# Performance work log

Measured on AMD Instinct MI355X. Metric: run time of the kernel, lower is better.

## Reference

```python
import jax, jax.numpy as jnp
import numpy as np

N_E = 8192
E_DIM = 512
BETA = 0.25


def setup_inputs() -> dict:
    key = jax.random.key(0)
    k1, k2, k3, k4, k5 = jax.random.split(key, 5)
    B, C, T = 8, E_DIM, 1024
    z = jax.random.normal(k1, (B, C, T), dtype=jnp.float32)
    # domain ids: 0 (speech), 1 (music), 2 (audio), 3 (no restriction / else-branch)
    audio_domain = jax.random.randint(k2, (B,), 0, 4, dtype=jnp.int64)
    # frozen codebook, init N(0, e_dim^-0.5) as in nn.init.normal_
    emb_weight = jax.random.normal(k3, (N_E, E_DIM), dtype=jnp.float32) * (E_DIM ** -0.5)
    # embedding_proj = nn.Linear(e_dim, e_dim): weight [out,in], bias [out]
    lim = 1.0 / np.sqrt(E_DIM)
    proj_w = jax.random.uniform(k4, (E_DIM, E_DIM), minval=-lim, maxval=lim, dtype=jnp.float32)
    proj_b = jax.random.uniform(k5, (E_DIM,), minval=-lim, maxval=lim, dtype=jnp.float32)
    return {"z": z, "audio_domain": audio_domain, "n_q": 1,
            "emb_weight": emb_weight, "proj_w": proj_w, "proj_b": proj_b}


def _domain_valid_mask(audio_domain):
    # valid[b, n] = True if code n is allowed for sample b
    cs = N_E // 4
    idx = jnp.arange(N_E)                      # [n_e]
    dom = audio_domain[:, None]                # [B, 1]
    m0 = idx < cs                              # domain 0: first quarter
    m1 = (idx >= cs) & (idx < 2 * cs)          # domain 1: second quarter
    m2 = idx >= 2 * cs                         # domain 2: last half
    valid = jnp.where(dom == 0, m0[None, :],
            jnp.where(dom == 1, m1[None, :],
            jnp.where(dom == 2, m2[None, :], True)))
    return valid                               # [B, n_e] bool


def reference(z, audio_domain, n_q, emb_weight, proj_w, proj_b):
    B, C, T = z.shape
    zt = jnp.transpose(z, (0, 2, 1))                       # [B, T, e_dim]
    zf = zt.reshape(-1, E_DIM)                              # [B*T, e_dim]
    # quant_codebook = Linear(embedding.weight)
    codebook = emb_weight @ proj_w.T + proj_b               # [n_e, e_dim]
    # squared euclidean distances via sum-sq + matmul
    d = (jnp.sum(zf * zf, axis=1, keepdims=True)
         + jnp.sum(codebook * codebook, axis=1)[None, :]
         - 2.0 * jnp.einsum('bd,nd->bn', zf, codebook))     # [B*T, n_e]
    d = d.reshape(B, T, N_E)
    valid = _domain_valid_mask(audio_domain)                # [B, n_e]
    d = jnp.where(valid[:, None, :], d, jnp.inf)
    min_idx = jnp.argmin(d, axis=2)                         # [B, T]
    z_q = codebook[min_idx]                                 # [B, T, e_dim]
    sg = jax.lax.stop_gradient
    # legacy=True commit loss
    commit_loss = (jnp.mean((sg(z_q) - zt) ** 2)
                   + BETA * jnp.mean((z_q - sg(zt)) ** 2))
    z_q = zt + sg(z_q - zt)                                 # straight-through
    z_q = jnp.transpose(z_q, (0, 2, 1))                     # [B, e_dim, T]
    min_idx = min_idx.reshape(1, B, T)                      # sane_index_shape
    return z_q, min_idx, commit_loss
```

## Files before the change

kernel.cpp:

```cpp
#include <hip/hip_runtime.h>
#include <math.h>

#define NE   8192
#define ED   512
#define BB   8
#define TT   1024
#define MM   (BB*TT)

#define FLT_BIG 3.402823466e38f
#define MARGIN  0.08f

typedef _Float16 half8 __attribute__((ext_vector_type(8)));
typedef _Float16 half4 __attribute__((ext_vector_type(4)));
typedef float    floatx4 __attribute__((ext_vector_type(4)));

typedef __attribute__((address_space(3))) unsigned int       lds_u32;
typedef const __attribute__((address_space(1))) unsigned int gbl_u32;

__device__ __forceinline__ void async_copy16(void* lds, const void* g) {
    __builtin_amdgcn_global_load_lds((gbl_u32*)(unsigned long long)g,
                                     (lds_u32*)(unsigned long long)lds,
                                     16, 0, 0);
}

__global__ __launch_bounds__(256) void k_prep(
    const float* __restrict__ z, const float* __restrict__ emb,
    const float* __restrict__ pw, _Float16* __restrict__ Zh,
    float* __restrict__ Zt, _Float16* __restrict__ Eb,
    _Float16* __restrict__ Wb, float* __restrict__ cnorm)
{
    const int bid = blockIdx.x;
    const int tid = threadIdx.x;
    if (bid < 1024) {
        __shared__ float T[64][68];
        const int ct = bid & 7, tt = (bid >> 3) & 15, b = bid >> 7;
        const int f4 = tid & 15;
        const int c0 = tid >> 4;
#pragma unroll
        for (int r = 0; r < 4; ++r) {
            const int c = c0 + r * 16;
            const float4 v = *(const float4*)(z + ((size_t)(b * ED + ct * 64 + c)) * TT + tt * 64 + f4 * 4);
            T[f4*4+0][c] = v.x; T[f4*4+1][c] = v.y;
            T[f4*4+2][c] = v.z; T[f4*4+3][c] = v.w;
        }
        __syncthreads();
        {
            const int tl = tid >> 2, q = tid & 3;
            const size_t m = (size_t)b * TT + tt * 64 + tl;
            _Float16* outh = Zh + m * 512 + ct * 64 + q * 16;
#pragma unroll
            for (int g = 0; g < 2; ++g) {
                half8 hv;
#pragma unroll
                for (int jj = 0; jj < 8; ++jj)
                    hv[jj] = (_Float16)(4.0f * T[tl][q*16 + g*8 + jj]);
                *(half8*)(outh + g * 8) = hv;
            }
        }
        {
            const int tl2 = tid >> 4;
            const int c4 = (tid & 15) * 4;
#pragma unroll
            for (int it = 0; it < 4; ++it) {
                const int t_local = tl2 + it * 16;
                const float4 v = *(const float4*)&T[t_local][c4];
                *(float4*)(Zt + ((size_t)b * TT + tt * 64 + t_local) * 512 + ct * 64 + c4) = v;
            }
        }
    } else if (bid < 5376) {
        const int g = (bid - 1024) * 256 + tid;
        const int row = g >> 7, c4 = (g & 127) * 4;
        const float* src;
        _Float16* dst;
        if (row < NE) { src = emb + (size_t)row * 512;        dst = Eb + (size_t)row * 1024; }
        else          { src = pw + (size_t)(row - NE) * 512;  dst = Wb + (size_t)(row - NE) * 1024; }
        const float4 v = *(const float4*)(src + c4);
        half4 h, l;
        const float s[4] = {v.x * 64.0f, v.y * 64.0f, v.z * 64.0f, v.w * 64.0f};
#pragma unroll
        for (int j = 0; j < 4; ++j) {
            const _Float16 hh = (_Float16)s[j];
            h[j] = hh;
            l[j] = (_Float16)(s[j] - (float)hh);
        }
        *(half4*)(dst + c4) = h;
        *(half4*)(dst + 512 + c4) = l;
    } else {
        const int zidx = bid - 5376;
        if (zidx < 8) {
            ((float4*)cnorm)[zidx * 256 + tid] = make_float4(0.f, 0.f, 0.f, 0.f);
        } else if (tid == 0) {
            cnorm[NE] = 0.0f;
            ((unsigned int*)cnorm)[NE + 1] = 0u;
        }
    }
}

#define S_AH 0
#define S_AL 8192
#define S_BH 16384
#define S_BL 20480
__global__ __launch_bounds__(256) void k_cb(
    const _Float16* __restrict__ Eb, const _Float16* __restrict__ Wb,
    const float* __restrict__ pb, float* __restrict__ cb,
    _Float16* __restrict__ Ch, float* __restrict__ cnorm)
{
    __shared__ __align__(16) _Float16 S[24576];

    const int tid = threadIdx.x;
    const int wave = tid >> 6, lane = tid & 63;
    const int n0 = blockIdx.x * 128, d0 = blockIdx.y * 64;
    const int wm = wave >> 1, wn = wave & 1;
    const int lm = lane & 15, lq = lane >> 4;

    floatx4 acc[4][2];
#pragma unroll
    for (int i = 0; i < 4; ++i)
#pragma unroll
        for (int j = 0; j < 2; ++j) acc[i][j] = (floatx4)0.0f;

    for (int lc = 0; lc < 8; ++lc) {
        const int kc = lc * 64;
        __syncthreads();
#pragma unroll
        for (int r = 0; r < 12; ++r) {
            const int s = wave * 12 + r;
            const int row8 = lane >> 3;
            const int srcx = lane & 7;
            if (s < 16) {
                const int row = s * 8 + row8;
                const int src = srcx ^ (row & 7);
                async_copy16(&S[S_AH + s * 512], Eb + (size_t)(n0 + row) * 1024 + kc + src * 8);
            } else if (s < 32) {
                const int s2 = s - 16;
                const int row = s2 * 8 + row8;
                const int src = srcx ^ (row & 7);
                async_copy16(&S[S_AL + s2 * 512], Eb + (size_t)(n0 + row) * 1024 + 512 + kc + src * 8);
            } else if (s < 40) {
                const int s2 = s - 32;
                const int row = s2 * 8 + row8;
                const int src = srcx ^ (row & 7);
                async_copy16(&S[S_BH + s2 * 512], Wb + (size_t)(d0 + row) * 1024 + kc + src * 8);
            } else {
                const int s2 = s - 40;
                const int row = s2 * 8 + row8;
                const int src = srcx ^ (row & 7);
                async_copy16(&S[S_BL + s2 * 512], Wb + (size_t)(d0 + row) * 1024 + 512 + kc + src * 8);
            }
        }
        __syncthreads();

#pragma unroll
        for (int ks = 0; ks < 2; ++ks) {
            half8 ah[4], al[4], bh[2], bl[2];
#pragma unroll
            for (int i = 0; i < 4; ++i) {
                const int row = wm * 64 + i * 16 + lm;
                const int slot = (ks * 4 + lq) ^ (row & 7);
                ah[i] = *(const half8*)&S[S_AH + row * 64 + slot * 8];
                al[i] = *(const half8*)&S[S_AL + row * 64 + slot * 8];
            }
#pragma unroll
            for (int j = 0; j < 2; ++j) {
                const int row = wn * 32 + j * 16 + lm;
                const int slot = (ks * 4 + lq) ^ (row & 7);
                bh[j] = *(const half8*)&S[S_BH + row * 64 + slot * 8];
                bl[j] = *(const half8*)&S[S_BL + row * 64 + slot * 8];
            }
#pragma unroll
            for (int i = 0; i < 4; ++i)
#pragma unroll
                for (int j = 0; j < 2; ++j) {
                    acc[i][j] = __builtin_amdgcn_mfma_f32_16x16x32_f16(ah[i], bh[j], acc[i][j], 0, 0, 0);
                    acc[i][j] = __builtin_amdgcn_mfma_f32_16x16x32_f16(ah[i], bl[j], acc[i][j], 0, 0, 0);
                    acc[i][j] = __builtin_amdgcn_mfma_f32_16x16x32_f16(al[i], bh[j], acc[i][j], 0, 0, 0);
                }
        }
    }

    float bias[2];
#pragma unroll
    for (int j = 0; j < 2; ++j) bias[j] = pb[d0 + wn * 32 + j * 16 + lm];

    float nsum[16];
#pragma unroll
    for (int p = 0; p < 16; ++p) nsum[p] = 0.0f;

#pragma unroll
    for (int i = 0; i < 4; ++i) {
#pragma unroll
        for (int j = 0; j < 2; ++j) {
            const int d = d0 + wn * 32 + j * 16 + lm;
#pragma unroll
            for (int r = 0; r < 4; ++r) {
                const float v = acc[i][j][r] * 0.000244140625f + bias[j];
                const int n = n0 + wm * 64 + i * 16 + lq * 4 + r;
                cb[(size_t)n * 512 + d] = v;
                Ch[(size_t)n * 512 + d] = (_Float16)(v * 64.0f);
                nsum[i * 4 + r] += v * v;
            }
        }
    }
#pragma unroll
    for (int stp = 1; stp < 16; stp <<= 1) {
#pragma unroll
        for (int p = 0; p < 16; ++p) nsum[p] += __shfl_xor(nsum[p], stp);
    }
    float myv = nsum[0];
#pragma unroll
    for (int p = 1; p < 16; ++p) if (lm == p) myv = nsum[p];
    const int n = n0 + wm * 64 + (lm >> 2) * 16 + lq * 4 + (lm & 3);
    atomicAdd(&cnorm[n], myv);
}

__global__ __launch_bounds__(256) void k_coarse(
    const _Float16* __restrict__ Zh, const _Float16* __restrict__ Ch,
    const float* __restrict__ cnorm, const int* __restrict__ dom_arr,
    _Float16* __restrict__ bmin)
{
    const int f   = blockIdx.y * 64 + blockIdx.x;
    const int xcd = f & 7;
    const int idx = f >> 3;
    const int mt  = idx >> 3;
    const int nt  = (idx & 7) * 8 + xcd;
    const int b = mt >> 3;
    const int dom = dom_arr[b];
    const int chunk = nt >> 4;
    const bool valid = (dom == 3) || (dom == 0 && chunk == 0) ||
                       (dom == 1 && chunk == 1) || (dom == 2 && chunk >= 2);
    if (!valid) return;

    const int tid = threadIdx.x;
    const int m0 = mt * 128, n0 = nt * 128;

    __shared__ __align__(16) _Float16 As[2][128 * 64];
    __shared__ __align__(16) _Float16 Bs[2][128 * 64];
    __shared__ __align__(16) float cnLds[128];

    const int wave = tid >> 6, lane = tid & 63;
    const int wm = wave >> 1, wn = wave & 1;
    const int lm = lane & 15, lq = lane >> 4;

    floatx4 acc[4][4];
#pragma unroll
    for (int i = 0; i < 4; ++i)
#pragma unroll
        for (int j = 0; j < 4; ++j) acc[i][j] = (floatx4)0.0f;

#define STAGE_K(buf, lc_) do {                                                  \
        const int kk0_ = (lc_) * 64;                                            \
        _Pragma("unroll")                                                       \
        for (int r_ = 0; r_ < 4; ++r_) {                                        \
            const int s_ = wave * 4 + r_;                                       \
            const int row_ = s_ * 8 + (lane >> 3);                              \
            const int src_ = (lane & 7) ^ (row_ & 7);                           \
            async_copy16(&As[buf][s_ * 512], Ch + (size_t)(n0 + row_) * 512 + kk0_ + src_ * 8); \
            async_copy16(&Bs[buf][s_ * 512], Zh + (size_t)(m0 + row_) * 512 + kk0_ + src_ * 8); \
        } } while (0)

    STAGE_K(0, 0);
    if (wave == 0 && lane < 32)
        async_copy16(&cnLds[0], cnorm + n0 + lane * 4);

    for (int lc = 0; lc < 8; ++lc) {
        const int cur = lc & 1;
        if (lc < 7) {
            STAGE_K(cur ^ 1, lc + 1);
            asm volatile("s_waitcnt vmcnt(8)" ::: "memory");
        } else {
            asm volatile("s_waitcnt vmcnt(0)" ::: "memory");
        }
        __builtin_amdgcn_s_barrier();
        asm volatile("" ::: "memory");

        __builtin_amdgcn_s_setprio(1);
#pragma unroll
        for (int ks = 0; ks < 2; ++ks) {
            half8 af[4], bf[4];
#pragma unroll
            for (int i = 0; i < 4; ++i) {
                const int row = wm * 64 + i * 16 + lm;
                const int slot = (ks * 4 + lq) ^ (row & 7);
                af[i] = *(const half8*)&As[cur][row * 64 + slot * 8];
            }
#pragma unroll
            for (int j = 0; j < 4; ++j) {
                const int row = wn * 64 + j * 16 + lm;
                const int slot = (ks * 4 + lq) ^ (row & 7);
                bf[j] = *(const half8*)&Bs[cur][row * 64 + slot * 8];
            }
#pragma unroll
            for (int i = 0; i < 4; ++i)
#pragma unroll
                for (int j = 0; j < 4; ++j)
                    acc[i][j] = __builtin_amdgcn_mfma_f32_16x16x32_f16(af[i], bf[j], acc[i][j], 0, 0, 0);
        }
        __builtin_amdgcn_s_setprio(0);
        asm volatile("" ::: "memory");
        __builtin_amdgcn_s_barrier();
    }
#undef STAGE_K

    float cnv[4][4];
#pragma unroll
    for (int i = 0; i < 4; ++i)
#pragma unroll
        for (int r = 0; r < 4; ++r)
            cnv[i][r] = cnLds[wm * 64 + i * 16 + lq * 4 + r];

    float um[4][4];
#pragma unroll
    for (int i = 0; i < 4; ++i) {
#pragma unroll
        for (int j = 0; j < 4; ++j) {
            float m01 = fminf(cnv[i][0] - acc[i][j][0] * 0.0078125f,
                              cnv[i][1] - acc[i][j][1] * 0.0078125f);
            float m23 = fminf(cnv[i][2] - acc[i][j][2] * 0.0078125f,
                              cnv[i][3] - acc[i][j][3] * 0.0078125f);
            um[i][j] = fminf(m01, m23);
        }
    }

    _Float16 (*bs)[40] = (_Float16(*)[40])&As[0][0];
#pragma unroll
    for (int i = 0; i < 4; ++i)
#pragma unroll
        for (int j = 0; j < 4; ++j)
            bs[wn * 64 + j * 16 + lm][wm * 16 + i * 4 + lq] = (_Float16)um[i][j];
    __syncthreads();
    {
        const int r = tid >> 1, h = tid & 1;
        half8 v0, v1;
#pragma unroll
        for (int k = 0; k < 8; ++k) { v0[k] = bs[r][h * 16 + k]; v1[k] = bs[r][h * 16 + 8 + k]; }
        _Float16* dst = bmin + (size_t)(m0 + r) * 2048 + nt * 32 + h * 16;
        *(half8*)dst = v0;
        *(half8*)(dst + 8) = v1;
    }
}

__global__ __launch_bounds__(256) void k_refine(
    const float* __restrict__ Zt, const float* __restrict__ cb,
    const float* __restrict__ cnorm, const _Float16* __restrict__ bmin,
    const int* __restrict__ dom_arr, int* __restrict__ minidx,
    float* __restrict__ out_idx)
{
    const int m = blockIdx.x * 4 + (threadIdx.x >> 6);
    const int lane = threadIdx.x & 63;
    const int b = m >> 10;
    const int dom = dom_arr[b];
    const int bg = (dom == 0) ? 0 : (dom == 1) ? 1 : (dom == 2) ? 2 : 0;
    const int ng = (dom == 2) ? 2 : (dom == 3) ? 4 : 1;

    const _Float16* brow = bmin + (size_t)m * 2048;
    float um[4][8];
    for (int g = 0; g < ng; ++g) {
        const half8 u = *(const half8*)(brow + (bg + g) * 512 + lane * 8);
#pragma unroll
        for (int j = 0; j < 8; ++j) um[g][j] = (float)u[j];
    }

    float gmin = FLT_BIG;
    for (int g = 0; g < ng; ++g)
#pragma unroll
        for (int j = 0; j < 8; ++j) gmin = fminf(gmin, um[g][j]);
#pragma unroll
    for (int s = 32; s > 0; s >>= 1) gmin = fminf(gmin, __shfl_xor(gmin, s));
    const float thr = gmin + MARGIN;

    float zr[8];
#pragma unroll
    for (int j = 0; j < 8; ++j)
        zr[j] = Zt[(size_t)m * 512 + lane + 64 * j];

    float bestv = FLT_BIG; int besti = 0x7FFFFFFF;

    for (int g = 0; g < ng; ++g) {
#pragma unroll
        for (int j = 0; j < 8; ++j) {
            unsigned long long mask = __ballot(um[g][j] <= thr);
            while (mask) {
                const int L = __ffsll(mask) - 1;
                mask &= mask - 1;
                const int unit = (bg + g) * 512 + L * 8 + j;
                const int nbase = unit * 4;
#pragma unroll
                for (int q = 0; q < 4; q += 2) {
                    const float* r0 = cb + (size_t)(nbase + q) * 512 + lane;
                    const float* r1 = r0 + 512;
                    float d0 = 0.f, d1 = 0.f;
#pragma unroll
                    for (int jj = 0; jj < 8; ++jj) {
                        d0 += zr[jj] * r0[64 * jj];
                        d1 += zr[jj] * r1[64 * jj];
                    }
#pragma unroll
                    for (int s = 32; s > 0; s >>= 1) {
                        d0 += __shfl_xor(d0, s);
                        d1 += __shfl_xor(d1, s);
                    }
                    const float f0 = cnorm[nbase + q]     - 2.0f * d0;
                    const float f1 = cnorm[nbase + q + 1] - 2.0f * d1;
                    const int n0i = nbase + q, n1i = nbase + q + 1;
                    if (f0 < bestv || (f0 == bestv && n0i < besti)) { bestv = f0; besti = n0i; }
                    if (f1 < bestv || (f1 == bestv && n1i < besti)) { bestv = f1; besti = n1i; }
                }
            }
        }
    }
    if (lane == 0) {
        minidx[m] = besti;
        out_idx[m] = (float)besti;
    }
}

#define ZQ_BLOCKS (4*16*8)
__global__ __launch_bounds__(256) void k_zq(
    const float* __restrict__ z, const float* __restrict__ cb,
    const int* __restrict__ minidx, float* __restrict__ outz,
    float* __restrict__ lossacc, unsigned int* __restrict__ donecnt,
    float* __restrict__ outloss)
{
    __shared__ float red[4];
    const int cc = blockIdx.x, tt = blockIdx.y, b = blockIdx.z;
    const int tl = threadIdx.x & 63;
    const int cg = threadIdx.x >> 6;
    const int t = tt * 64 + tl;
    const int idx = minidx[b * TT + t];
    const float* __restrict__ crow = cb + (size_t)idx * 512;

    float lsum = 0.f;
#pragma unroll 8
    for (int k = 0; k < 32; ++k) {
        const int c = cc * 128 + cg + k * 4;
        const float cv = crow[c];
        const size_t off = ((size_t)(b * ED + c)) * TT + t;
        const float zv = z[off];
        const float d = cv - zv;
        lsum += d * d;
        outz[off] = cv;
    }
#pragma unroll
    for (int off = 32; off > 0; off >>= 1) lsum += __shfl_down(lsum, off);
    if (tl == 0) red[threadIdx.x >> 6] = lsum;
    __syncthreads();
    if (threadIdx.x == 0) {
        atomicAdd(lossacc, red[0] + red[1] + red[2] + red[3]);
        __threadfence();
        const unsigned int old = atomicAdd(donecnt, 1u);
        if (old == ZQ_BLOCKS - 1) {
            const float total = atomicAdd(lossacc, 0.0f);
            *outloss = 1.25f * total / (float)(BB * ED * TT);
        }
    }
}

extern "C" void kernel_launch(void* const* d_in, const int* in_sizes, int n_in,
                              void* d_out, int out_size, void* d_ws, size_t ws_size,
                              hipStream_t stream)
{
    const float* z   = (const float*)d_in[0];
    const int*   dom = (const int*)d_in[1];
    const float* emb = (const float*)d_in[3];
    const float* pw  = (const float*)d_in[4];
    const float* pb  = (const float*)d_in[5];
    float* out = (float*)d_out;

    char* p = (char*)d_ws;
    _Float16* Zh = (_Float16*)p;            p += (size_t)MM * 512 * 2;
    float*    Zt = (float*)p;               p += (size_t)MM * 512 * 4;
    _Float16* Eb = (_Float16*)p;            p += (size_t)NE * 1024 * 2;
    _Float16* Wb = (_Float16*)p;            p += (size_t)ED * 1024 * 2;
    float*    cb = (float*)p;               p += (size_t)NE * 512 * 4;
    _Float16* Ch = (_Float16*)p;            p += (size_t)NE * 512 * 2;
    float* cnorm = (float*)p;               p += (size_t)NE * 4;
    float* lossacc = (float*)p;             p += 4;
    unsigned int* donecnt = (unsigned int*)p; p += 4;
    _Float16* bmin = (_Float16*)p;          p += (size_t)MM * 2048 * 2;
    int*   minidx = (int*)p;

    k_prep   <<<1024 + (NE + ED) / 2 + 9, 256, 0, stream>>>(z, emb, pw, Zh, Zt, Eb, Wb, cnorm);
    k_cb     <<<dim3(64, 8), 256, 0, stream>>>(Eb, Wb, pb, cb, Ch, cnorm);
    k_coarse <<<dim3(64, 64), 256, 0, stream>>>(Zh, Ch, cnorm, dom, bmin);
    k_refine <<<MM / 4, 256, 0, stream>>>(Zt, cb, cnorm, bmin, dom, minidx, out + (size_t)NE * ED);
    k_zq     <<<dim3(4, 16, 8), 256, 0, stream>>>(z, cb, minidx, out, lossacc, donecnt,
                                                  out + (size_t)NE * ED + MM);
}
```

Baseline: 210.8 us.

## Enlarge coarse distance GEMM tile to 256x256 with 8-wave phased pipeline

The coarse fp16 distance GEMM now uses 256x256 output tiles with 512 threads (8 waves, 2x4 layout) instead of 128x128 tiles with 4 waves. The K loop is split into four phases that interleave LDS fragment reads, async global-to-LDS staging of the next K slice, and MFMA bursts, separated by barriers. The aim is to cut global and LDS traffic per FLOP through more operand reuse and to overlap loads with compute. In exchange it uses about 129KB of LDS and more accumulator registers per wave, which limits occupancy to roughly one block per CU and adds more barriers per iteration. The bmin epilogue is rewritten to match the new per-tile layout.

New measurement: 271.8 us. +28.9%, slower.

```diff
diff --git a/kernel.cpp b/kernel.cpp
--- a/kernel.cpp
+++ b/kernel.cpp
@@ -21,6 +21,12 @@
     __builtin_amdgcn_global_load_lds((gbl_u32*)(unsigned long long)g,
                                      (lds_u32*)(unsigned long long)lds,
                                      16, 0, 0);
+}
+
+__device__ __forceinline__ void bar() {
+    asm volatile("" ::: "memory");
+    __builtin_amdgcn_s_barrier();
+    asm volatile("" ::: "memory");
 }
 
 __global__ __launch_bounds__(256) void k_prep(
@@ -213,104 +219,156 @@
     atomicAdd(&cnorm[n], myv);
 }
 
-__global__ __launch_bounds__(256) void k_coarse(
+__global__ __launch_bounds__(512) void k_coarse(
     const _Float16* __restrict__ Zh, const _Float16* __restrict__ Ch,
     const float* __restrict__ cnorm, const int* __restrict__ dom_arr,
     _Float16* __restrict__ bmin)
 {
-    const int f   = blockIdx.y * 64 + blockIdx.x;
+    const int f   = blockIdx.y * 32 + blockIdx.x;
     const int xcd = f & 7;
     const int idx = f >> 3;
-    const int mt  = idx >> 3;
-    const int nt  = (idx & 7) * 8 + xcd;
-    const int b = mt >> 3;
+    const int mt  = idx >> 2;
+    const int nt  = (idx & 3) * 8 + xcd;
+    const int b   = mt >> 2;
     const int dom = dom_arr[b];
-    const int chunk = nt >> 4;
+    const int chunk = nt >> 3;
     const bool valid = (dom == 3) || (dom == 0 && chunk == 0) ||
                        (dom == 1 && chunk == 1) || (dom == 2 && chunk >= 2);
     if (!valid) return;
 
     const int tid = threadIdx.x;
-    const int m0 = mt * 128, n0 = nt * 128;
-
-    __shared__ __align__(16) _Float16 As[2][128 * 64];
-    __shared__ __align__(16) _Float16 Bs[2][128 * 64];
-    __shared__ __align__(16) float cnLds[128];
+    const int m0 = mt * 256, n0 = nt * 256;
+
+    __shared__ __align__(16) _Float16 S[2][2][256 * 64];
+    __shared__ __align__(16) float cnLds[256];
 
     const int wave = tid >> 6, lane = tid & 63;
-    const int wm = wave >> 1, wn = wave & 1;
+    const int wm = wave >> 2, wn = wave & 3;
     const int lm = lane & 15, lq = lane >> 4;
 
-    floatx4 acc[4][4];
-#pragma unroll
-    for (int i = 0; i < 4; ++i)
+    floatx4 acc[8][4];
+#pragma unroll
+    for (int i = 0; i < 8; ++i)
 #pragma unroll
         for (int j = 0; j < 4; ++j) acc[i][j] = (floatx4)0.0f;
 
-#define STAGE_K(buf, lc_) do {                                                  \
-        const int kk0_ = (lc_) * 64;                                            \
-        _Pragma("unroll")                                                       \
-        for (int r_ = 0; r_ < 4; ++r_) {                                        \
-            const int s_ = wave * 4 + r_;                                       \
-            const int row_ = s_ * 8 + (lane >> 3);                              \
-            const int src_ = (lane & 7) ^ (row_ & 7);                           \
-            async_copy16(&As[buf][s_ * 512], Ch + (size_t)(n0 + row_) * 512 + kk0_ + src_ * 8); \
-            async_copy16(&Bs[buf][s_ * 512], Zh + (size_t)(m0 + row_) * 512 + kk0_ + src_ * 8); \
+#define STAGE_HALF(buf, X, h, kt_) do {                                          \
+        const int kk0_ = (kt_) * 64;                                             \
+        _Pragma("unroll")                                                        \
+        for (int r_ = 0; r_ < 2; ++r_) {                                         \
+            const int s_   = wave * 2 + r_;                                      \
+            const int row_ = (h) * 128 + s_ * 8 + (lane >> 3);                   \
+            const int src_ = (lane & 7) ^ (row_ & 7);                            \
+            const _Float16* gp_ = (X) ? (Zh + (size_t)(m0 + row_) * 512 + kk0_ + src_ * 8)  \
+                                      : (Ch + (size_t)(n0 + row_) * 512 + kk0_ + src_ * 8); \
+            async_copy16(&S[buf][X][((h) * 16 + s_) * 512], gp_);                \
         } } while (0)
 
-    STAGE_K(0, 0);
-    if (wave == 0 && lane < 32)
+    STAGE_HALF(0, 0, 0, 0); STAGE_HALF(0, 0, 1, 0);
+    STAGE_HALF(0, 1, 0, 0); STAGE_HALF(0, 1, 1, 0);
+    if (wave == 0)
         async_copy16(&cnLds[0], cnorm + n0 + lane * 4);
-
-    for (int lc = 0; lc < 8; ++lc) {
-        const int cur = lc & 1;
-        if (lc < 7) {
-            STAGE_K(cur ^ 1, lc + 1);
-            asm volatile("s_waitcnt vmcnt(8)" ::: "memory");
-        } else {
+    asm volatile("s_waitcnt vmcnt(0)" ::: "memory");
+    bar();
+
+#pragma unroll 2
+    for (int kt = 0; kt < 8; ++kt) {
+        const int cur = kt & 1;
+        const int nxt = cur ^ 1;
+        half8 af[4], bf[4];
+
+#pragma unroll
+        for (int jj = 0; jj < 4; ++jj) {
+            const int row = wn * 64 + jj * 16 + lm;
+            const int slot = lq ^ (row & 7);
+            bf[jj] = *(const half8*)&S[cur][1][row * 64 + slot * 8];
+        }
+#pragma unroll
+        for (int ii = 0; ii < 4; ++ii) {
+            const int row = wm * 128 + ii * 16 + lm;
+            const int slot = lq ^ (row & 7);
+            af[ii] = *(const half8*)&S[cur][0][row * 64 + slot * 8];
+        }
+        if (kt < 7) { STAGE_HALF(nxt, 0, 0, kt + 1); STAGE_HALF(nxt, 0, 1, kt + 1); }
+        bar();
+        __builtin_amdgcn_s_setprio(1);
+#pragma unroll
+        for (int ii = 0; ii < 4; ++ii)
+#pragma unroll
+            for (int jj = 0; jj < 4; ++jj)
+                acc[ii][jj] = __builtin_amdgcn_mfma_f32_16x16x32_f16(af[ii], bf[jj], acc[ii][jj], 0, 0, 0);
+        __builtin_amdgcn_s_setprio(0);
+        bar();
+
+#pragma unroll
+        for (int ii = 0; ii < 4; ++ii) {
+            const int row = wm * 128 + (ii + 4) * 16 + lm;
+            const int slot = lq ^ (row & 7);
+            af[ii] = *(const half8*)&S[cur][0][row * 64 + slot * 8];
+        }
+        if (kt < 7) { STAGE_HALF(nxt, 1, 0, kt + 1); STAGE_HALF(nxt, 1, 1, kt + 1); }
+        bar();
+        __builtin_amdgcn_s_setprio(1);
+#pragma unroll
+        for (int ii = 0; ii < 4; ++ii)
+#pragma unroll
+            for (int jj = 0; jj < 4; ++jj)
+                acc[ii + 4][jj] = __builtin_amdgcn_mfma_f32_16x16x32_f16(af[ii], bf[jj], acc[ii + 4][jj], 0, 0, 0);
+        __builtin_amdgcn_s_setprio(0);
+        bar();
+
+#pragma unroll
+        for (int jj = 0; jj < 4; ++jj) {
+            const int row = wn * 64 + jj * 16 + lm;
+            const int slot = (4 + lq) ^ (row & 7);
+            bf[jj] = *(const half8*)&S[cur][1][row * 64 + slot * 8];
+        }
+#pragma unroll
+        for (int ii = 0; ii < 4; ++ii) {
+            const int row = wm * 128 + ii * 16 + lm;
+            const int slot = (4 + lq) ^ (row & 7);
+            af[ii] = *(const half8*)&S[cur][0][row * 64 + slot * 8];
+        }
+        bar();
+        __builtin_amdgcn_s_setprio(1);
+#pragma unroll
+        for (int ii = 0; ii < 4; ++ii)
+#pragma unroll
+            for (int jj = 0; jj < 4; ++jj)
+                acc[ii][jj] = __builtin_amdgcn_mfma_f32_16x16x32_f16(af[ii], bf[jj], acc[ii][jj], 0, 0, 0);
+        __builtin_amdgcn_s_setprio(0);
+        bar();
+
+#pragma unroll
+        for (int ii = 0; ii < 4; ++ii) {
+            const int row = wm * 128 + (ii + 4) * 16 + lm;
+            const int slot = (4 + lq) ^ (row & 7);
+            af[ii] = *(const half8*)&S[cur][0][row * 64 + slot * 8];
+        }
+        bar();
+        __builtin_amdgcn_s_setprio(1);
+#pragma unroll
+        for (int ii = 0; ii < 4; ++ii)
+#pragma unroll
+            for (int jj = 0; jj < 4; ++jj)
+                acc[ii + 4][jj] = __builtin_amdgcn_mfma_f32_16x16x32_f16(af[ii], bf[jj], acc[ii + 4][jj], 0, 0, 0);
+        __builtin_amdgcn_s_setprio(0);
+        if (kt < 7)
             asm volatile("s_waitcnt vmcnt(0)" ::: "memory");
-        }
-        __builtin_amdgcn_s_barrier();
-        asm volatile("" ::: "memory");
-
-        __builtin_amdgcn_s_setprio(1);
-#pragma unroll
-        for (int ks = 0; ks < 2; ++ks) {
-            half8 af[4], bf[4];
-#pragma unroll
-            for (int i = 0; i < 4; ++i) {
-                const int row = wm * 64 + i * 16 + lm;
-                const int slot = (ks * 4 + lq) ^ (row & 7);
-                af[i] = *(const half8*)&As[cur][row * 64 + slot * 8];
-            }
-#pragma unroll
-            for (int j = 0; j < 4; ++j) {
-                const int row = wn * 64 + j * 16 + lm;
-                const int slot = (ks * 4 + lq) ^ (row & 7);
-                bf[j] = *(const half8*)&Bs[cur][row * 64 + slot * 8];
-            }
-#pragma unroll
-            for (int i = 0; i < 4; ++i)
-#pragma unroll
-                for (int j = 0; j < 4; ++j)
-                    acc[i][j] = __builtin_amdgcn_mfma_f32_16x16x32_f16(af[i], bf[j], acc[i][j], 0, 0, 0);
-        }
-        __builtin_amdgcn_s_setprio(0);
-        asm volatile("" ::: "memory");
-        __builtin_amdgcn_s_barrier();
-    }
-#undef STAGE_K
-
-    float cnv[4][4];
-#pragma unroll
-    for (int i = 0; i < 4; ++i)
+        bar();
+    }
+#undef STAGE_HALF
+
+    float cnv[8][4];
+#pragma unroll
+    for (int i = 0; i < 8; ++i)
 #pragma unroll
         for (int r = 0; r < 4; ++r)
-            cnv[i][r] = cnLds[wm * 64 + i * 16 + lq * 4 + r];
-
-    float um[4][4];
-#pragma unroll
-    for (int i = 0; i < 4; ++i) {
+            cnv[i][r] = cnLds[wm * 128 + i * 16 + lq * 4 + r];
+
+    float um[8][4];
+#pragma unroll
+    for (int i = 0; i < 8; ++i) {
 #pragma unroll
         for (int j = 0; j < 4; ++j) {
             float m01 = fminf(cnv[i][0] - acc[i][j][0] * 0.0078125f,
@@ -321,21 +379,23 @@
         }
     }
 
-    _Float16 (*bs)[40] = (_Float16(*)[40])&As[0][0];
-#pragma unroll
-    for (int i = 0; i < 4; ++i)
+    _Float16 (*bs)[68] = (_Float16(*)[68])&S[0][0][0];
+#pragma unroll
+    for (int i = 0; i < 8; ++i)
 #pragma unroll
         for (int j = 0; j < 4; ++j)
-            bs[wn * 64 + j * 16 + lm][wm * 16 + i * 4 + lq] = (_Float16)um[i][j];
+            bs[wn * 64 + j * 16 + lm][wm * 32 + i * 4 + lq] = (_Float16)um[i][j];
     __syncthreads();
     {
         const int r = tid >> 1, h = tid & 1;
-        half8 v0, v1;
-#pragma unroll
-        for (int k = 0; k < 8; ++k) { v0[k] = bs[r][h * 16 + k]; v1[k] = bs[r][h * 16 + 8 + k]; }
-        _Float16* dst = bmin + (size_t)(m0 + r) * 2048 + nt * 32 + h * 16;
-        *(half8*)dst = v0;
-        *(half8*)(dst + 8) = v1;
+        half8 v[4];
+#pragma unroll
+        for (int k = 0; k < 4; ++k)
+#pragma unroll
+            for (int e = 0; e < 8; ++e) v[k][e] = bs[r][h * 32 + k * 8 + e];
+        _Float16* dst = bmin + (size_t)(m0 + r) * 2048 + nt * 64 + h * 32;
+#pragma unroll
+        for (int k = 0; k < 4; ++k) *(half8*)(dst + k * 8) = v[k];
     }
 }
 
@@ -481,7 +541,7 @@
 
     k_prep   <<<1024 + (NE + ED) / 2 + 9, 256, 0, stream>>>(z, emb, pw, Zh, Zt, Eb, Wb, cnorm);
     k_cb     <<<dim3(64, 8), 256, 0, stream>>>(Eb, Wb, pb, cb, Ch, cnorm);
-    k_coarse <<<dim3(64, 64), 256, 0, stream>>>(Zh, Ch, cnorm, dom, bmin);
+    k_coarse <<<dim3(32, 32), 512, 0, stream>>>(Zh, Ch, cnorm, dom, bmin);
     k_refine <<<MM / 4, 256, 0, stream>>>(Zt, cb, cnorm, bmin, dom, minidx, out + (size_t)NE * ED);
     k_zq     <<<dim3(4, 16, 8), 256, 0, stream>>>(z, cb, minidx, out, lossacc, donecnt,
                                                   out + (size_t)NE * ED + MM);
```
